# Optimization experiments

Hardware: AMD Instinct MI355X
Metric: run time of the kernel (lower is better)

Reference implementation:

```python
import jax, jax.numpy as jnp
import numpy as np

B, T, D, U = 32, 2048, 1024, 1024

def setup_inputs() -> dict:
    key = jax.random.key(0)
    ks = jax.random.split(key, 8)
    s = 0.02
    return {
        "query": jax.random.normal(ks[0], (B, D), dtype=jnp.float32),
        "values": jax.random.normal(ks[1], (B, T, D), dtype=jnp.float32),
        "W1": jax.random.normal(ks[2], (D, U), dtype=jnp.float32) * s,
        "b1": jnp.zeros((U,), dtype=jnp.float32),
        "W2": jax.random.normal(ks[3], (D, U), dtype=jnp.float32) * s,
        "b2": jnp.zeros((U,), dtype=jnp.float32),
        "V": jax.random.normal(ks[4], (U, 1), dtype=jnp.float32) * s,
        "bv": jnp.zeros((1,), dtype=jnp.float32),
    }

def reference(query, values, W1, b1, W2, b2, V, bv):
    # query: [B, D] -> [B, 1, U] via W2; values: [B, T, D] -> [B, T, U] via W1
    q_proj = query @ W2 + b2                     # [B, U]
    v_proj = jnp.einsum('btd,du->btu', values, W1) + b1   # [B, T, U]
    # score: Dense(1) on tanh(sum) -> [B, T, 1]
    score = jnp.tanh(v_proj + q_proj[:, None, :]) @ V + bv  # [B, T, 1]
    attention_weights = jax.nn.softmax(score, axis=1)        # softmax over time
    context_vector = jnp.sum(attention_weights * values, axis=1)  # [B, D]
    return context_vector, attention_weights
```

## Files before the change

### kernel.cpp

```cpp
#include <hip/hip_runtime.h>
#include <hip/hip_bf16.h>
#include <stdint.h>

#define WS_W1F   0
#define WS_QP2   2097152
#define WS_ESC   (WS_QP2 + 131072)
#define WS_PCTX  (WS_ESC + 262144)
#define WS_PDEN  (WS_PCTX + 4194304)
#define WS_NEED  (WS_PDEN + 4096)

typedef __attribute__((ext_vector_type(8))) short bf16x8;
typedef __attribute__((ext_vector_type(4))) float f32x4;

__device__ inline uint16_t f2b(float f) {
    __hip_bfloat16 h = __float2bfloat16(f);
    return *reinterpret_cast<uint16_t*>(&h);
}

__global__ __launch_bounds__(256) void k_prep(const float* __restrict__ W1,
                                              const float* __restrict__ query,
                                              const float* __restrict__ W2,
                                              const float* __restrict__ b1,
                                              const float* __restrict__ b2,
                                              __hip_bfloat16* __restrict__ W1f,
                                              float* __restrict__ qp2,
                                              float* __restrict__ zctx,
                                              float* __restrict__ zden) {
    __shared__ float qs[1024];
    __shared__ float part[4][64];
    int blk = blockIdx.x, tid = threadIdx.x;
    if (blk < 256) {
        int lane = tid & 63, fi = tid >> 6;
        int l15 = lane & 15, quad = lane >> 4;
        #pragma unroll
        for (int p = 0; p < 2; ++p) {
            int frag = blk * 8 + p * 4 + fi;
            int ut = frag >> 5, ks = frag & 31;
            union { uint16_t h[8]; int4 v; } pk;
            #pragma unroll
            for (int j = 0; j < 8; ++j) {
                float x = W1[(size_t)(ks * 32 + quad * 8 + j) * 1024 + ut * 16 + l15];
                pk.h[j] = f2b(x);
            }
            *(int4*)((char*)W1f + (size_t)frag * 1024 + lane * 16) = pk.v;
        }
    } else {
        int bq = blk - 256;
        int b = bq >> 4, us = bq & 15, u0 = us * 64;
        if (zctx != nullptr && us == 0) {
            *(float4*)(zctx + b * 1024 + tid * 4) = make_float4(0.f, 0.f, 0.f, 0.f);
            if (b == 0 && tid < 32) zden[tid] = 0.f;
        }
        const float* q = query + b * 1024;
        #pragma unroll
        for (int i = 0; i < 4; ++i) qs[i * 256 + tid] = q[i * 256 + tid];
        __syncthreads();
        int ul = tid & 63, g = tid >> 6;
        float a = 0.f;
        const float* w2p = W2 + (size_t)(g * 256) * 1024 + u0 + ul;
        const float* qg = qs + g * 256;
        #pragma unroll 8
        for (int d = 0; d < 256; ++d)
            a += qg[d] * w2p[(size_t)d * 1024];
        part[g][ul] = a;
        __syncthreads();
        if (tid < 64) {
            float r = part[0][tid] + part[1][tid] + part[2][tid] + part[3][tid]
                    + b1[u0 + tid] + b2[u0 + tid];
            qp2[b * 1024 + u0 + tid] = r;
        }
    }
}

__global__ __launch_bounds__(512, 1) void k_score(
        const float* __restrict__ values, const __hip_bfloat16* __restrict__ W1f,
        const float* __restrict__ qp2, const float* __restrict__ V,
        float* __restrict__ escore, float* __restrict__ pctx,
        float* __restrict__ pden, float* __restrict__ ctxa) {
    extern __shared__ char smem[];
    float* red = (float*)(smem + 65536);

    const int tid = threadIdx.x;
    const int lane = tid & 63, w = tid >> 6;
    const int quad = lane >> 4, l15 = lane & 15;
    const int b = blockIdx.x >> 5, trow0 = (blockIdx.x & 31) << 6;
    const int rot = blockIdx.x & 7;

    const float* Ag = values + (size_t)(b * 2048 + trow0) * 1024;

    const int crow = tid >> 5, sc = tid & 31;
    const int pos_w = (sc & 16) | ((sc & 15) ^ crow);
    const float* sgbase = Ag + (size_t)crow * 1024 + sc * 8;
    char* wbase = smem + crow * 512 + pos_w * 16;

    const char* Bbase = (const char*)W1f + (size_t)(w * 8) * 32768 + lane * 16;

    f32x4 acc[4][8];
    #pragma unroll
    for (int rt = 0; rt < 4; ++rt)
        #pragma unroll
        for (int ct = 0; ct < 8; ++ct) acc[rt][ct] = (f32x4){0.f, 0.f, 0.f, 0.f};

    bf16x8 bfr[2][8];

    #pragma unroll
    for (int s = 0; s < 4; ++s) {
        float4 v0 = *(const float4*)(sgbase + s * 16384);
        float4 v1 = *(const float4*)(sgbase + s * 16384 + 4);
        union { uint16_t h[8]; int4 v; } pk;
        pk.h[0]=f2b(v0.x); pk.h[1]=f2b(v0.y); pk.h[2]=f2b(v0.z); pk.h[3]=f2b(v0.w);
        pk.h[4]=f2b(v1.x); pk.h[5]=f2b(v1.y); pk.h[6]=f2b(v1.z); pk.h[7]=f2b(v1.w);
        *(int4*)(wbase + s * 8192) = pk.v;
    }
    #pragma unroll
    for (int ct = 0; ct < 8; ++ct)
        bfr[0][ct] = *(const bf16x8*)(Bbase + (size_t)(ct * 32 + rot) * 1024);
    asm volatile("s_waitcnt lgkmcnt(0)" ::: "memory");
    __builtin_amdgcn_s_barrier();
    __builtin_amdgcn_sched_barrier(0);

    #pragma unroll
    for (int q = 0; q < 4; ++q) {
        const int abuf = q & 1;
        #pragma unroll
        for (int ksl = 0; ksl < 8; ++ksl) {
            const int it = q * 8 + ksl;
            const int curb = it & 1;
            const bool do_stage = (q < 3) && (ksl < 4);
            float4 sv0, sv1;
            if (do_stage) {
                const float* sp = sgbase + ksl * 16384 + (q + 1) * 256;
                sv0 = *(const float4*)sp;
                sv1 = *(const float4*)(sp + 4);
            }
            const int lc = (ksl + rot) & 7;
            const int cbi = lc * 4 + quad;
            const int posr = (cbi & 16) | ((cbi & 15) ^ l15);
            bf16x8 af[4];
            #pragma unroll
            for (int rt = 0; rt < 4; ++rt)
                af[rt] = *(bf16x8*)(smem + abuf * 32768 + (rt * 16 + l15) * 512 + posr * 16);
            if (it < 31) {
                const int nq = (ksl == 7) ? q + 1 : q;
                const int nlc = (ksl + 1 + rot) & 7;
                const int nkg = nq * 8 + nlc;
                #pragma unroll
                for (int ct = 0; ct < 8; ++ct)
                    bfr[curb ^ 1][ct] =
                        *(const bf16x8*)(Bbase + (size_t)(ct * 32 + nkg) * 1024);
            }
            __builtin_amdgcn_sched_barrier(0);
            __builtin_amdgcn_s_setprio(1);
            #pragma unroll
            for (int ct = 0; ct < 4; ++ct)
                #pragma unroll
                for (int rt = 0; rt < 4; ++rt)
                    acc[rt][ct] = __builtin_amdgcn_mfma_f32_16x16x32_bf16(
                        af[rt], bfr[curb][ct], acc[rt][ct], 0, 0, 0);
            __builtin_amdgcn_s_setprio(0);
            __builtin_amdgcn_sched_barrier(0);
            __builtin_amdgcn_s_setprio(1);
            #pragma unroll
            for (int ct = 4; ct < 8; ++ct)
                #pragma unroll
                for (int rt = 0; rt < 4; ++rt)
                    acc[rt][ct] = __builtin_amdgcn_mfma_f32_16x16x32_bf16(
                        af[rt], bfr[curb][ct], acc[rt][ct], 0, 0, 0);
            __builtin_amdgcn_s_setprio(0);
            __builtin_amdgcn_sched_barrier(0);
            if (do_stage) {
                union { uint16_t h[8]; int4 v; } pk;
                pk.h[0]=f2b(sv0.x); pk.h[1]=f2b(sv0.y); pk.h[2]=f2b(sv0.z); pk.h[3]=f2b(sv0.w);
                pk.h[4]=f2b(sv1.x); pk.h[5]=f2b(sv1.y); pk.h[6]=f2b(sv1.z); pk.h[7]=f2b(sv1.w);
                *(int4*)(wbase + (abuf ^ 1) * 32768 + ksl * 8192) = pk.v;
            }
        }
        if (q < 3) {
            asm volatile("s_waitcnt lgkmcnt(0)" ::: "memory");
            __builtin_amdgcn_s_barrier();
            __builtin_amdgcn_sched_barrier(0);
        }
    }

    float srow[4][4];
    #pragma unroll
    for (int rt = 0; rt < 4; ++rt)
        #pragma unroll
        for (int r = 0; r < 4; ++r) srow[rt][r] = 0.f;
    #pragma unroll
    for (int ct = 0; ct < 8; ++ct) {
        int u = w * 128 + ct * 16 + l15;
        float qv = qp2[b * 1024 + u];
        float vv = V[u];
        #pragma unroll
        for (int rt = 0; rt < 4; ++rt)
            #pragma unroll
            for (int r = 0; r < 4; ++r) {
                float x = acc[rt][ct][r] + qv;
                float e = __expf(2.f * x);
                float t = 1.f - 2.f * __builtin_amdgcn_rcpf(1.f + e);
                srow[rt][r] += t * vv;
            }
    }

    #pragma unroll
    for (int rt = 0; rt < 4; ++rt)
        #pragma unroll
        for (int r = 0; r < 4; ++r) {
            float s = srow[rt][r];
            s += __shfl_xor(s, 1, 64);
            s += __shfl_xor(s, 2, 64);
            s += __shfl_xor(s, 4, 64);
            s += __shfl_xor(s, 8, 64);
            srow[rt][r] = s;
        }
    if (l15 == 0) {
        #pragma unroll
        for (int rt = 0; rt < 4; ++rt)
            #pragma unroll
            for (int r = 0; r < 4; ++r)
                red[w * 64 + rt * 16 + quad * 4 + r] = srow[rt][r];
    }
    __syncthreads();

    float* wl = (float*)smem;
    if (tid < 64) {
        float s = 0.f;
        #pragma unroll
        for (int k = 0; k < 8; ++k) s += red[k * 64 + tid];
        float e = __expf(s);
        escore[b * 2048 + trow0 + tid] = e;
        wl[tid] = e;
        float dsum = e;
        #pragma unroll
        for (int off = 32; off; off >>= 1) dsum += __shfl_xor(dsum, off, 64);
        if (tid == 0) {
            if (pctx != nullptr) pden[blockIdx.x] = dsum;
            else                 atomicAdd(&pden[b], dsum);
        }
    }
    __syncthreads();

    {
        const float* Vg = values + (size_t)(b * 2048 + trow0) * 1024 + tid * 2;
        float ax = 0.f, ay = 0.f;
        #pragma unroll 8
        for (int t = 0; t < 64; ++t) {
            float wv = wl[t];
            float2 v = *(const float2*)(Vg + (size_t)t * 1024);
            ax += wv * v.x; ay += wv * v.y;
        }
        if (pctx != nullptr) {
            *(float2*)(pctx + (size_t)blockIdx.x * 1024 + tid * 2) = make_float2(ax, ay);
        } else {
            float* o = ctxa + b * 1024 + tid * 2;
            atomicAdd(o + 0, ax);
            atomicAdd(o + 1, ay);
        }
    }
}

__global__ __launch_bounds__(256) void k_final(const float* __restrict__ pctx,
                                               const float* __restrict__ pden,
                                               const float* __restrict__ escore,
                                               float* __restrict__ out) {
    __shared__ float sinv;
    int b = blockIdx.x, tid = threadIdx.x;
    if (tid == 0) {
        float dsum = 0.f;
        if (pctx != nullptr) {
            #pragma unroll
            for (int t = 0; t < 32; ++t) dsum += pden[b * 32 + t];
        } else {
            dsum = pden[b];
        }
        sinv = 1.f / dsum;
    }
    __syncthreads();
    float inv = sinv;

    int d = tid * 4;
    if (pctx != nullptr) {
        float4 a = {0.f, 0.f, 0.f, 0.f};
        #pragma unroll 8
        for (int t = 0; t < 32; ++t) {
            float4 p = *(const float4*)(pctx + (size_t)(b * 32 + t) * 1024 + d);
            a.x += p.x; a.y += p.y; a.z += p.z; a.w += p.w;
        }
        a.x *= inv; a.y *= inv; a.z *= inv; a.w *= inv;
        *(float4*)(out + b * 1024 + d) = a;
    } else {
        float4 a = *(const float4*)(out + b * 1024 + d);
        a.x *= inv; a.y *= inv; a.z *= inv; a.w *= inv;
        *(float4*)(out + b * 1024 + d) = a;
    }

    #pragma unroll
    for (int i = 0; i < 8; ++i) {
        int t = i * 256 + tid;
        out[32768 + b * 2048 + t] = escore[b * 2048 + t] * inv;
    }
}

extern "C" void kernel_launch(void* const* d_in, const int* in_sizes, int n_in,
                              void* d_out, int out_size, void* d_ws, size_t ws_size,
                              hipStream_t stream) {
    const float* query  = (const float*)d_in[0];
    const float* values = (const float*)d_in[1];
    const float* W1 = (const float*)d_in[2];
    const float* b1 = (const float*)d_in[3];
    const float* W2 = (const float*)d_in[4];
    const float* b2 = (const float*)d_in[5];
    const float* V  = (const float*)d_in[6];

    char* ws = (char*)d_ws;
    __hip_bfloat16* W1f = (__hip_bfloat16*)(ws + WS_W1F);
    float* qp2 = (float*)(ws + WS_QP2);
    float* out = (float*)d_out;

    const bool big = ws_size >= (size_t)WS_NEED;
    float* escore = big ? (float*)(ws + WS_ESC)  : out + 32768;
    float* pctx   = big ? (float*)(ws + WS_PCTX) : nullptr;
    float* pden   = big ? (float*)(ws + WS_PDEN) : (float*)(ws + WS_ESC);
    float* zctx   = big ? nullptr : out;
    float* zden   = big ? nullptr : pden;

    (void)hipFuncSetAttribute((const void*)k_score,
                              hipFuncAttributeMaxDynamicSharedMemorySize, 67584);

    k_prep<<<768, 256, 0, stream>>>(W1, query, W2, b1, b2, W1f, qp2, zctx, zden);
    k_score<<<1024, 512, 67584, stream>>>(values, W1f, qp2, V, escore, pctx, pden, out);
    k_final<<<32, 256, 0, stream>>>(pctx, pden, escore, out);
}
```

Before: 519.8 us.

## Split query projection across more blocks with atomics and stagger k-slice order per wave

The query·W2 projection is repartitioned into many more blocks, each covering a 128-wide d slice, with partial sums accumulated into qp2 via atomicAdd after a new init kernel seeds the biases and zeroes the accumulators. This gives the prep stage more parallelism and shorter serial loops, at the cost of an extra kernel launch and atomic traffic. In the score kernel, each wave now starts its k-slice loop at a different offset (wave index plus block-derived rotation). This is meant to spread W1f global reads and LDS bank accesses across waves.

```diff
diff --git a/kernel.cpp b/kernel.cpp
--- a/kernel.cpp
+++ b/kernel.cpp
@@ -17,17 +17,29 @@
     return *reinterpret_cast<uint16_t*>(&h);
 }
 
+__global__ __launch_bounds__(256) void k_init(const float* __restrict__ b1,
+                                              const float* __restrict__ b2,
+                                              float* __restrict__ qp2,
+                                              float* __restrict__ zctx,
+                                              float* __restrict__ zden) {
+    int b = blockIdx.x, tid = threadIdx.x;
+    #pragma unroll
+    for (int i = 0; i < 4; ++i) {
+        int u = i * 256 + tid;
+        qp2[b * 1024 + u] = b1[u] + b2[u];
+    }
+    if (zctx != nullptr) {
+        *(float4*)(zctx + b * 1024 + tid * 4) = make_float4(0.f, 0.f, 0.f, 0.f);
+        if (b == 0 && tid < 32) zden[tid] = 0.f;
+    }
+}
+
 __global__ __launch_bounds__(256) void k_prep(const float* __restrict__ W1,
                                               const float* __restrict__ query,
                                               const float* __restrict__ W2,
-                                              const float* __restrict__ b1,
-                                              const float* __restrict__ b2,
                                               __hip_bfloat16* __restrict__ W1f,
-                                              float* __restrict__ qp2,
-                                              float* __restrict__ zctx,
-                                              float* __restrict__ zden) {
-    __shared__ float qs[1024];
-    __shared__ float part[4][64];
+                                              float* __restrict__ qp2) {
+    __shared__ float qs[128];
     int blk = blockIdx.x, tid = threadIdx.x;
     if (blk < 256) {
         int lane = tid & 63, fi = tid >> 6;
@@ -45,30 +57,20 @@
             *(int4*)((char*)W1f + (size_t)frag * 1024 + lane * 16) = pk.v;
         }
     } else {
-        int bq = blk - 256;
-        int b = bq >> 4, us = bq & 15, u0 = us * 64;
-        if (zctx != nullptr && us == 0) {
-            *(float4*)(zctx + b * 1024 + tid * 4) = make_float4(0.f, 0.f, 0.f, 0.f);
-            if (b == 0 && tid < 32) zden[tid] = 0.f;
-        }
-        const float* q = query + b * 1024;
-        #pragma unroll
-        for (int i = 0; i < 4; ++i) qs[i * 256 + tid] = q[i * 256 + tid];
+        int j = blk - 256;
+        int b = j >> 6, rem = j & 63;
+        int uq = rem >> 3, dq = rem & 7;
+        if (tid < 128) qs[tid] = query[b * 1024 + dq * 128 + tid];
         __syncthreads();
-        int ul = tid & 63, g = tid >> 6;
+        int ul = tid & 127, dh = tid >> 7;
+        int u = uq * 128 + ul;
+        const float* w2p = W2 + (size_t)(dq * 128 + dh * 64) * 1024 + u;
+        const float* qg = qs + dh * 64;
         float a = 0.f;
-        const float* w2p = W2 + (size_t)(g * 256) * 1024 + u0 + ul;
-        const float* qg = qs + g * 256;
         #pragma unroll 8
-        for (int d = 0; d < 256; ++d)
+        for (int d = 0; d < 64; ++d)
             a += qg[d] * w2p[(size_t)d * 1024];
-        part[g][ul] = a;
-        __syncthreads();
-        if (tid < 64) {
-            float r = part[0][tid] + part[1][tid] + part[2][tid] + part[3][tid]
-                    + b1[u0 + tid] + b2[u0 + tid];
-            qp2[b * 1024 + u0 + tid] = r;
-        }
+        atomicAdd(&qp2[b * 1024 + u], a);
     }
 }
 
@@ -84,7 +86,8 @@
     const int lane = tid & 63, w = tid >> 6;
     const int quad = lane >> 4, l15 = lane & 15;
     const int b = blockIdx.x >> 5, trow0 = (blockIdx.x & 31) << 6;
-    const int rot = blockIdx.x & 7;
+    const int rot = (blockIdx.x >> 3) & 7;
+    const int ph = (w + rot) & 7;
 
     const float* Ag = values + (size_t)(b * 2048 + trow0) * 1024;
 
@@ -112,9 +115,12 @@
         pk.h[4]=f2b(v1.x); pk.h[5]=f2b(v1.y); pk.h[6]=f2b(v1.z); pk.h[7]=f2b(v1.w);
         *(int4*)(wbase + s * 8192) = pk.v;
     }
-    #pragma unroll
-    for (int ct = 0; ct < 8; ++ct)
-        bfr[0][ct] = *(const bf16x8*)(Bbase + (size_t)(ct * 32 + rot) * 1024);
+    {
+        const int kg0 = ph;
+        #pragma unroll
+        for (int ct = 0; ct < 8; ++ct)
+            bfr[0][ct] = *(const bf16x8*)(Bbase + (size_t)(ct * 32 + kg0) * 1024);
+    }
     asm volatile("s_waitcnt lgkmcnt(0)" ::: "memory");
     __builtin_amdgcn_s_barrier();
     __builtin_amdgcn_sched_barrier(0);
@@ -133,7 +139,7 @@
                 sv0 = *(const float4*)sp;
                 sv1 = *(const float4*)(sp + 4);
             }
-            const int lc = (ksl + rot) & 7;
+            const int lc = (ksl + ph) & 7;
             const int cbi = lc * 4 + quad;
             const int posr = (cbi & 16) | ((cbi & 15) ^ l15);
             bf16x8 af[4];
@@ -142,8 +148,8 @@
                 af[rt] = *(bf16x8*)(smem + abuf * 32768 + (rt * 16 + l15) * 512 + posr * 16);
             if (it < 31) {
                 const int nq = (ksl == 7) ? q + 1 : q;
-                const int nlc = (ksl + 1 + rot) & 7;
-                const int nkg = nq * 8 + nlc;
+                const int nksl = (ksl == 7) ? 0 : ksl + 1;
+                const int nkg = nq * 8 + ((nksl + ph) & 7);
                 #pragma unroll
                 for (int ct = 0; ct < 8; ++ct)
                     bfr[curb ^ 1][ct] =
@@ -328,7 +334,8 @@
     (void)hipFuncSetAttribute((const void*)k_score,
                               hipFuncAttributeMaxDynamicSharedMemorySize, 67584);
 
-    k_prep<<<768, 256, 0, stream>>>(W1, query, W2, b1, b2, W1f, qp2, zctx, zden);
+    k_init<<<32, 256, 0, stream>>>(b1, b2, qp2, zctx, zden);
+    k_prep<<<2304, 256, 0, stream>>>(W1, query, W2, W1f, qp2);
     k_score<<<1024, 512, 67584, stream>>>(values, W1f, qp2, V, escore, pctx, pden, out);
     k_final<<<32, 256, 0, stream>>>(pctx, pden, escore, out);
 }
```

New measurement: 505.7 us. 2.7% less time.
